# Kernel tuning notes

Measured on AMD Instinct MI355X. Metric: run time of the kernel, lower is better.

The kernel has to match this reference:

```python
import jax, jax.numpy as jnp
import numpy as np
import math

D_MODEL = 1024
N_HEADS = 16
N_QUBITS = 8
HEAD_DIM = D_MODEL // N_HEADS
B, L = 2, 2048


def setup_inputs() -> dict:
    key = jax.random.key(0)
    ks = jax.random.split(key, 16)
    s = 0.02
    return {
        "query": jax.random.normal(ks[0], (B, L, D_MODEL), jnp.float32),
        "key_": jax.random.normal(ks[1], (B, L, D_MODEL), jnp.float32),
        "value": jax.random.normal(ks[2], (B, L, D_MODEL), jnp.float32),
        "Wq": jax.random.normal(ks[3], (D_MODEL, D_MODEL), jnp.float32) * s,
        "bq": jnp.zeros((D_MODEL,), jnp.float32),
        "Wk": jax.random.normal(ks[4], (D_MODEL, D_MODEL), jnp.float32) * s,
        "bk": jnp.zeros((D_MODEL,), jnp.float32),
        "Wv": jax.random.normal(ks[5], (D_MODEL, D_MODEL), jnp.float32) * s,
        "bv": jnp.zeros((D_MODEL,), jnp.float32),
        "Wo": jax.random.normal(ks[6], (D_MODEL, D_MODEL), jnp.float32) * s,
        "bo": jnp.zeros((D_MODEL,), jnp.float32),
        "Wf": jax.random.normal(ks[7], (HEAD_DIM, N_QUBITS), jnp.float32) * s,  # feature map weight (input->qubits)
        "bf": jnp.zeros((N_QUBITS,), jnp.float32),
        "quantum_weights": jax.random.normal(ks[8], (N_HEADS, N_QUBITS), jnp.float32) * 0.1,
        "entanglement_strength": jnp.asarray(0.5, jnp.float32),
    }


def _heads(x):
    # [B, L, D] -> [B, H, L, head_dim]
    b, l, _ = x.shape
    return x.reshape(b, l, N_HEADS, HEAD_DIM).transpose(0, 2, 1, 3)


def reference(query, key_, value, Wq, bq, Wk, bk, Wv, bv, Wo, bo, Wf, bf, quantum_weights, entanglement_strength):
    Qh = _heads(query @ Wq.T + bq)   # [B,H,L,d]
    Kh = _heads(key_ @ Wk.T + bk)
    Vh = _heads(value @ Wv.T + bv)

    classical = jnp.einsum("bhid,bhjd->bhij", Qh, Kh) / math.sqrt(HEAD_DIM)

    # quantum feature map: tanh(linear) -> [B,H,L,Q]
    qq = jnp.tanh(jnp.einsum("bhld,dq->bhlq", Qh, Wf) + bf)
    kq = jnp.tanh(jnp.einsum("bhld,dq->bhlq", Kh, Wf) + bf)

    # mean_q w_q*cos(qq_i - kq_j) == (1/Q)[(w*cos qq)@cos(kq)^T + (w*sin qq)@sin(kq)^T]
    w = jax.nn.sigmoid(quantum_weights)[None, :, None, :]  # [1,H,1,Q]
    quantum = (
        jnp.einsum("bhiq,bhjq->bhij", jnp.cos(qq) * w, jnp.cos(kq))
        + jnp.einsum("bhiq,bhjq->bhij", jnp.sin(qq) * w, jnp.sin(kq))
    ) / N_QUBITS
    ent = jax.nn.sigmoid(entanglement_strength)
    quantum = quantum * ent

    mix = ent  # same sigmoid(entanglement_strength) used as mixing weight
    combined = (1.0 - mix) * classical + mix * quantum

    attn = jax.nn.softmax(combined, axis=-1)  # [B,H,L,L]
    attended = jnp.einsum("bhij,bhjd->bhid", attn, Vh)
    attended = attended.transpose(0, 2, 1, 3).reshape(query.shape[0], query.shape[1], D_MODEL)
    output = attended @ Wo.T + bo
    return output, attn.mean(axis=1)
```

## Files before the change

### kernel.cpp

```cpp
#include <hip/hip_runtime.h>


typedef unsigned short u16;
typedef unsigned int u32;
typedef short v8s __attribute__((ext_vector_type(8)));
typedef float v4f __attribute__((ext_vector_type(4)));

static __device__ __forceinline__ float b2f(u16 h) {
  union { u32 u; float f; } a; a.u = ((u32)h) << 16; return a.f;
}
static __device__ __forceinline__ u16 f2b(float f) {
  union { float f; u32 u; } a; a.f = f;
  u32 u = a.u;
  u32 r = u + 0x7FFFu + ((u >> 16) & 1u);
  return (u16)(r >> 16);
}
static __device__ __forceinline__ u32 fbits(float f) {
  union { float f; u32 u; } a; a.f = f; return a.u;
}
static __device__ __forceinline__ v4f mfma16(v8s a, v8s b, v4f c) {
  return __builtin_amdgcn_mfma_f32_16x16x32_bf16(a, b, c, 0, 0, 0);
}
static __device__ __forceinline__ void gload16(const u16* g, u16* l) {
  __builtin_amdgcn_global_load_lds((const __attribute__((address_space(1))) u32*)g,
                                   (__attribute__((address_space(3))) u32*)l, 16, 0, 0);
}

__global__ __launch_bounds__(256) void k_f2b(const float* __restrict__ x, u16* __restrict__ y, int n4) {
  int i = blockIdx.x * 256 + threadIdx.x;
  if (i >= n4) return;
  float4 v = ((const float4*)x)[i];
  union { u16 s[4]; uint2 u; } o;
  o.s[0] = f2b(v.x); o.s[1] = f2b(v.y); o.s[2] = f2b(v.z); o.s[3] = f2b(v.w);
  ((uint2*)y)[i] = o.u;
}

__global__ __launch_bounds__(256) void k_gemm128(
    const u16* __restrict__ A0, const u16* __restrict__ A1, const u16* __restrict__ A2,
    const u16* __restrict__ B0, const u16* __restrict__ B1, const u16* __restrict__ B2,
    const float* __restrict__ bias0, const float* __restrict__ bias1, const float* __restrict__ bias2,
    u16* __restrict__ O0, u16* __restrict__ O1, u16* __restrict__ O2t,
    float* __restrict__ Cf) {
  __shared__ __align__(16) u16 As[128 * 32];
  __shared__ __align__(16) u16 Bs[128 * 32];
  __shared__ __align__(16) u16 Ts[4][64][68];
  const int K = 1024, N = 1024;
  int t = threadIdx.x, w = t >> 6, lane = t & 63, quad = lane >> 4, l16 = lane & 15;
  int z = blockIdx.z;
  const u16* A = (z == 0) ? A0 : (z == 1) ? A1 : A2;
  const u16* Bm = (z == 0) ? B0 : (z == 1) ? B1 : B2;
  const float* bias = (z == 0) ? bias0 : (z == 1) ? bias1 : bias2;
  int n0 = blockIdx.x * 128, m0 = blockIdx.y * 128;

  int srow = lane >> 2, scol = (lane & 3) * 8;
  const u16 *ga[2], *gb[2];
  u16 *la[2], *lbp[2];
#pragma unroll
  for (int p = 0; p < 2; ++p) {
    int row = p * 64 + w * 16 + srow;
    ga[p] = A + (size_t)(m0 + row) * K + scol;
    gb[p] = Bm + (size_t)(n0 + row) * K + scol;
    la[p] = As + (p * 256 + w * 64) * 8;
    lbp[p] = Bs + (p * 256 + w * 64) * 8;
  }

  int mrow = (w >> 1) * 64, ncol = (w & 1) * 64;
  v4f zf = {0.f, 0.f, 0.f, 0.f};
  v4f acc[4][4];
#pragma unroll
  for (int mi = 0; mi < 4; ++mi)
#pragma unroll
    for (int ni = 0; ni < 4; ++ni) acc[mi][ni] = zf;

  for (int k0 = 0; k0 < K; k0 += 32) {
    __syncthreads();
#pragma unroll
    for (int p = 0; p < 2; ++p) {
      gload16(ga[p] + k0, la[p]);
      gload16(gb[p] + k0, lbp[p]);
    }
    __syncthreads();
    v8s af[4], bfr[4];
#pragma unroll
    for (int x = 0; x < 4; ++x) {
      af[x] = *(const v8s*)&As[(mrow + x * 16 + l16) * 32 + quad * 8];
      bfr[x] = *(const v8s*)&Bs[(ncol + x * 16 + l16) * 32 + quad * 8];
    }
#pragma unroll
    for (int mi = 0; mi < 4; ++mi)
#pragma unroll
      for (int ni = 0; ni < 4; ++ni)
        acc[mi][ni] = mfma16(af[mi], bfr[ni], acc[mi][ni]);
  }

  float bv[4];
#pragma unroll
  for (int ni = 0; ni < 4; ++ni) bv[ni] = bias[n0 + ncol + ni * 16 + l16];

  if (Cf) {
#pragma unroll
    for (int mi = 0; mi < 4; ++mi)
#pragma unroll
      for (int ni = 0; ni < 4; ++ni)
#pragma unroll
        for (int r = 0; r < 4; ++r)
          Cf[(size_t)(m0 + mrow + mi * 16 + quad * 4 + r) * N + n0 + ncol + ni * 16 + l16] =
              acc[mi][ni][r] + bv[ni];
  } else if (z != 2) {
    u16* O = z ? O1 : O0;
#pragma unroll
    for (int mi = 0; mi < 4; ++mi)
#pragma unroll
      for (int ni = 0; ni < 4; ++ni)
#pragma unroll
        for (int r = 0; r < 4; ++r)
          O[(size_t)(m0 + mrow + mi * 16 + quad * 4 + r) * N + n0 + ncol + ni * 16 + l16] =
              f2b(acc[mi][ni][r] + bv[ni]);
  } else {
#pragma unroll
    for (int mi = 0; mi < 4; ++mi)
#pragma unroll
      for (int ni = 0; ni < 4; ++ni)
#pragma unroll
        for (int r = 0; r < 4; ++r)
          Ts[w][mi * 16 + quad * 4 + r][ni * 16 + l16] = f2b(acc[mi][ni][r] + bv[ni]);
    int c = lane;
    union { uint4 u[8]; u16 s[64]; } cb;
#pragma unroll
    for (int e = 0; e < 64; ++e) cb.s[e] = Ts[w][e][c];
    int bb = m0 >> 11, ml = m0 & 2047;
    u16* dst = O2t + ((size_t)(bb * 1024 + n0 + ncol + c)) * 2048 + ml + mrow;
#pragma unroll
    for (int e = 0; e < 8; ++e) *(uint4*)(dst + e * 8) = cb.u[e];
  }
}

__global__ __launch_bounds__(256) void k_features(const u16* __restrict__ P, const float* __restrict__ Wf,
                                                  const float* __restrict__ bff, const float* __restrict__ qw,
                                                  const float* __restrict__ entp, u16* __restrict__ Out, int isK) {
  int idx = blockIdx.x * 256 + threadIdx.x;
  int b = idx >> 15, h = (idx >> 11) & 15, l = idx & 2047;
  const u16* src = P + ((size_t)(b * 2048 + l)) * 1024 + h * 64;
  u16* dst = Out + (size_t)idx * 96;
  float x[64];
#pragma unroll
  for (int g = 0; g < 8; ++g) {
    union { uint4 u; u16 s[8]; } uu;
    uu.u = *(const uint4*)(src + g * 8);
#pragma unroll
    for (int e = 0; e < 8; ++e) x[g * 8 + e] = b2f(uu.s[e]);
  }
  float qv[8];
#pragma unroll
  for (int q = 0; q < 8; ++q) {
    float a = bff[q];
    for (int d = 0; d < 64; ++d) a += x[d] * Wf[d * 8 + q];
    qv[q] = tanhf(a);
  }
  float ent = 1.f / (1.f + __expf(-entp[0]));
  if (!isK) {
#pragma unroll
    for (int g = 0; g < 8; ++g) *(uint4*)(dst + g * 8) = *(const uint4*)(src + g * 8);
#pragma unroll
    for (int q = 0; q < 8; ++q) {
      float sw = 1.f / (1.f + __expf(-qw[h * 8 + q]));
      dst[64 + q] = f2b(cosf(qv[q]) * sw);
      dst[72 + q] = f2b(sinf(qv[q]) * sw);
    }
  } else {
    float c1 = (1.f - ent) * 0.125f, c2 = ent * ent * 0.125f;
#pragma unroll
    for (int d = 0; d < 64; ++d) dst[d] = f2b(x[d] * c1);
#pragma unroll
    for (int q = 0; q < 8; ++q) {
      dst[64 + q] = f2b(cosf(qv[q]) * c2);
      dst[72 + q] = f2b(sinf(qv[q]) * c2);
    }
  }
#pragma unroll
  for (int e = 80; e < 96; ++e) dst[e] = 0;
}

__global__ __launch_bounds__(256) void k_flash(const u16* __restrict__ Qa, const u16* __restrict__ Ka,
                                               const u16* __restrict__ VtG, u16* __restrict__ At,
                                               float* __restrict__ lb) {
  __shared__ __align__(16) u16 Ks[64][104];
  __shared__ __align__(16) u16 Vt[64][72];
  __shared__ __align__(16) u16 Ps[4][2][16][72];

  int t = threadIdx.x, w = t >> 6, lane = t & 63, quad = lane >> 4, l16 = lane & 15;
  int i0 = blockIdx.x * 128, h = blockIdx.y, b = blockIdx.z;
  size_t qbase = ((size_t)(b * 16 + h)) * 2048 * 96;
  v8s aq[2][3];
#pragma unroll
  for (int i16 = 0; i16 < 2; ++i16) {
    const u16* Qrow = Qa + qbase + (size_t)(i0 + w * 32 + i16 * 16 + l16) * 96;
#pragma unroll
    for (int ks = 0; ks < 3; ++ks) aq[i16][ks] = *(const v8s*)(Qrow + ks * 32 + quad * 8);
  }
  const u16* Kbase = Ka + qbase;
  const u16* Vbase = VtG + ((size_t)(b * 1024 + h * 64)) * 2048;

  const u16 *kg[3], *vg[2];
  u16 *kd[3], *vd[2];
#pragma unroll
  for (int p = 0; p < 3; ++p) {
    int idx = t + p * 256, r_ = idx / 12, c_ = idx % 12;
    kg[p] = Kbase + (size_t)r_ * 96 + c_ * 8;
    kd[p] = &Ks[r_][c_ * 8];
  }
#pragma unroll
  for (int p = 0; p < 2; ++p) {
    int idx = t + p * 256, d_ = idx >> 3, c_ = (idx & 7) * 8;
    vg[p] = Vbase + (size_t)d_ * 2048 + c_;
    vd[p] = &Vt[d_][c_];
  }

  v4f zf = {0.f, 0.f, 0.f, 0.f};
  v4f oacc[2][4];
#pragma unroll
  for (int i16 = 0; i16 < 2; ++i16)
#pragma unroll
    for (int d16 = 0; d16 < 4; ++d16) oacc[i16][d16] = zf;
  float l_acc[2] = {0.f, 0.f};

  uint4 fk0 = *(const uint4*)kg[0];
  uint4 fk1 = *(const uint4*)kg[1];
  uint4 fk2 = *(const uint4*)kg[2];
  uint4 fv0 = *(const uint4*)vg[0];
  uint4 fv1 = *(const uint4*)vg[1];

  for (int j0 = 0; j0 < 2048; j0 += 64) {
    *(uint4*)kd[0] = fk0;
    *(uint4*)kd[1] = fk1;
    *(uint4*)kd[2] = fk2;
    *(uint4*)vd[0] = fv0;
    *(uint4*)vd[1] = fv1;
    __syncthreads();
    kg[0] += 6144; kg[1] += 6144; kg[2] += 6144; vg[0] += 64; vg[1] += 64;
    if (j0 + 64 < 2048) {
      fk0 = *(const uint4*)kg[0];
      fk1 = *(const uint4*)kg[1];
      fk2 = *(const uint4*)kg[2];
      fv0 = *(const uint4*)vg[0];
      fv1 = *(const uint4*)vg[1];
    }

    v4f sacc[2][4];
#pragma unroll
    for (int i16 = 0; i16 < 2; ++i16)
#pragma unroll
      for (int j16 = 0; j16 < 4; ++j16) sacc[i16][j16] = zf;
#pragma unroll
    for (int j16 = 0; j16 < 4; ++j16)
#pragma unroll
      for (int ks = 0; ks < 3; ++ks) {
        v8s kf = *(const v8s*)&Ks[j16 * 16 + l16][ks * 32 + quad * 8];
        sacc[0][j16] = mfma16(kf, aq[0][ks], sacc[0][j16]);
        sacc[1][j16] = mfma16(kf, aq[1][ks], sacc[1][j16]);
      }

#pragma unroll
    for (int i16 = 0; i16 < 2; ++i16)
#pragma unroll
      for (int j16 = 0; j16 < 4; ++j16) {
        float e0 = __expf(sacc[i16][j16][0]);
        float e1 = __expf(sacc[i16][j16][1]);
        float e2 = __expf(sacc[i16][j16][2]);
        float e3 = __expf(sacc[i16][j16][3]);
        l_acc[i16] += (e0 + e1) + (e2 + e3);
        uint2 pp;
        pp.x = __builtin_amdgcn_perm(fbits(e1) + 0x8000u, fbits(e0) + 0x8000u, 0x07060302u);
        pp.y = __builtin_amdgcn_perm(fbits(e3) + 0x8000u, fbits(e2) + 0x8000u, 0x07060302u);
        *(uint2*)&Ps[w][i16][l16][j16 * 16 + quad * 4] = pp;
      }
#pragma unroll
    for (int jh = 0; jh < 2; ++jh) {
      v8s pf0 = *(const v8s*)&Ps[w][0][l16][jh * 32 + quad * 8];
      v8s pf1 = *(const v8s*)&Ps[w][1][l16][jh * 32 + quad * 8];
#pragma unroll
      for (int d16 = 0; d16 < 4; ++d16) {
        v8s vf = *(const v8s*)&Vt[d16 * 16 + l16][jh * 32 + quad * 8];
        oacc[0][d16] = mfma16(pf0, vf, oacc[0][d16]);
        oacc[1][d16] = mfma16(pf1, vf, oacc[1][d16]);
      }
    }
    __syncthreads();
  }

#pragma unroll
  for (int i16 = 0; i16 < 2; ++i16) {
    l_acc[i16] += __shfl_xor(l_acc[i16], 16, 64);
    l_acc[i16] += __shfl_xor(l_acc[i16], 32, 64);
    float linv = 1.f / l_acc[i16];
#pragma unroll
    for (int r = 0; r < 4; ++r) {
      float li = __shfl(linv, quad * 4 + r, 64);
      int ri = i0 + w * 32 + i16 * 16 + quad * 4 + r;
#pragma unroll
      for (int d16 = 0; d16 < 4; ++d16)
        At[((size_t)(b * 2048 + ri)) * 1024 + h * 64 + d16 * 16 + l16] = f2b(oacc[i16][d16][r] * li);
    }
    if (lane < 16) {
      size_t mbase = ((size_t)(b * 16 + h)) * 2048;
      lb[mbase + i0 + w * 32 + i16 * 16 + lane] = l_acc[i16];
    }
  }
}

__global__ __launch_bounds__(256) void k_pass2(const u16* __restrict__ Qa, const u16* __restrict__ Ka,
                                               const float* __restrict__ lb,
                                               float* __restrict__ out1) {
  __shared__ __align__(16) u16 Ks[64][104];
  __shared__ float Ls[16][128];
  int t = threadIdx.x, w = t >> 6, lane = t & 63, quad = lane >> 4, l16 = lane & 15;
  int j0 = blockIdx.x * 64, i0 = blockIdx.y * 128, b = blockIdx.z;

#pragma unroll
  for (int rep = 0; rep < 8; ++rep) {
    int idx = t + rep * 256;
    int hh = idx >> 7, il = idx & 127;
    Ls[hh][il] = 0.0625f / lb[((size_t)(b * 16 + hh)) * 2048 + i0 + il];
  }

  size_t base0 = (size_t)b * 16 * 2048 * 96;
  const u16* kg[3]; u16* kd[3];
#pragma unroll
  for (int rep = 0; rep < 3; ++rep) {
    int idx = t + rep * 256;
    int r_ = idx / 12, c_ = idx % 12;
    kg[rep] = Ka + base0 + (size_t)(j0 + r_) * 96 + c_ * 8;
    kd[rep] = &Ks[r_][c_ * 8];
  }
  uint4 f0 = *(const uint4*)kg[0];
  uint4 f1 = *(const uint4*)kg[1];
  uint4 f2 = *(const uint4*)kg[2];

  const u16* q0 = Qa + base0 + (size_t)(i0 + w * 32 + l16) * 96 + quad * 8;
  const u16* q1 = q0 + 16 * 96;

  v4f zf = {0.f, 0.f, 0.f, 0.f};
  v4f macc[2][4];
#pragma unroll
  for (int i16 = 0; i16 < 2; ++i16)
#pragma unroll
    for (int j16 = 0; j16 < 4; ++j16) macc[i16][j16] = zf;

  v8s a[2][3];
#pragma unroll
  for (int ks = 0; ks < 3; ++ks) {
    a[0][ks] = *(const v8s*)(q0 + ks * 32);
    a[1][ks] = *(const v8s*)(q1 + ks * 32);
  }

  for (int h = 0; h < 16; ++h) {
    *(uint4*)kd[0] = f0;
    *(uint4*)kd[1] = f1;
    *(uint4*)kd[2] = f2;
    __syncthreads();
    if (h < 15) {
      kg[0] += 196608; kg[1] += 196608; kg[2] += 196608;
      f0 = *(const uint4*)kg[0];
      f1 = *(const uint4*)kg[1];
      f2 = *(const uint4*)kg[2];
    }

    v4f sacc[2][4];
#pragma unroll
    for (int i16 = 0; i16 < 2; ++i16)
#pragma unroll
      for (int j16 = 0; j16 < 4; ++j16) sacc[i16][j16] = zf;
#pragma unroll
    for (int ks = 0; ks < 3; ++ks)
#pragma unroll
      for (int j16 = 0; j16 < 4; ++j16) {
        v8s kf = *(const v8s*)&Ks[j16 * 16 + l16][ks * 32 + quad * 8];
        sacc[0][j16] = mfma16(a[0][ks], kf, sacc[0][j16]);
        sacc[1][j16] = mfma16(a[1][ks], kf, sacc[1][j16]);
      }

    if (h < 15) {
      q0 += 196608; q1 += 196608;
#pragma unroll
      for (int ks = 0; ks < 3; ++ks) {
        a[0][ks] = *(const v8s*)(q0 + ks * 32);
        a[1][ks] = *(const v8s*)(q1 + ks * 32);
      }
    }

    float li[2][4];
#pragma unroll
    for (int i16 = 0; i16 < 2; ++i16)
#pragma unroll
      for (int r = 0; r < 4; ++r)
        li[i16][r] = Ls[h][w * 32 + i16 * 16 + quad * 4 + r];
#pragma unroll
    for (int i16 = 0; i16 < 2; ++i16)
#pragma unroll
      for (int j16 = 0; j16 < 4; ++j16)
#pragma unroll
        for (int r = 0; r < 4; ++r)
          macc[i16][j16][r] += __expf(sacc[i16][j16][r]) * li[i16][r];
    __syncthreads();
  }

  float* o = out1 + (size_t)b * 2048 * 2048;
#pragma unroll
  for (int i16 = 0; i16 < 2; ++i16)
#pragma unroll
    for (int j16 = 0; j16 < 4; ++j16)
#pragma unroll
      for (int r = 0; r < 4; ++r)
        o[(size_t)(i0 + w * 32 + i16 * 16 + quad * 4 + r) * 2048 + j0 + j16 * 16 + l16] =
            macc[i16][j16][r];
}

extern "C" void kernel_launch(void* const* d_in, const int* in_sizes, int n_in,
                              void* d_out, int out_size, void* d_ws, size_t ws_size,
                              hipStream_t stream) {
  (void)in_sizes; (void)n_in; (void)out_size; (void)ws_size;
  const float* query = (const float*)d_in[0];
  const float* key_  = (const float*)d_in[1];
  const float* value = (const float*)d_in[2];
  const float* Wq = (const float*)d_in[3];
  const float* bq = (const float*)d_in[4];
  const float* Wk = (const float*)d_in[5];
  const float* bk = (const float*)d_in[6];
  const float* Wv = (const float*)d_in[7];
  const float* bv = (const float*)d_in[8];
  const float* Wo = (const float*)d_in[9];
  const float* bo = (const float*)d_in[10];
  const float* Wf = (const float*)d_in[11];
  const float* bff = (const float*)d_in[12];
  const float* qw = (const float*)d_in[13];
  const float* entp = (const float*)d_in[14];

  char* p = (char*)d_ws;
  u16* Xq  = (u16*)(p + 0);
  u16* Xk  = (u16*)(p + 8388608);
  u16* Xv  = (u16*)(p + 16777216);
  u16* Wqb = (u16*)(p + 25165824);
  u16* Wkb = (u16*)(p + 27262976);
  u16* Wvb = (u16*)(p + 29360128);
  u16* Wob = (u16*)(p + 31457280);
  u16* Qp  = (u16*)(p + 33554432);
  u16* Kp  = (u16*)(p + 41943040);
  u16* VtG = (u16*)(p + 50331648);
  u16* Qaa = (u16*)(p + 58720256);
  u16* Kaa = (u16*)(p + 71303168);
  float* lb = (float*)(p + 84148224);
  u16* At  = (u16*)(p + 84410368);

  k_f2b<<<4096, 256, 0, stream>>>(query, Xq, 1048576);
  k_f2b<<<4096, 256, 0, stream>>>(key_,  Xk, 1048576);
  k_f2b<<<4096, 256, 0, stream>>>(value, Xv, 1048576);
  k_f2b<<<1024, 256, 0, stream>>>(Wq, Wqb, 262144);
  k_f2b<<<1024, 256, 0, stream>>>(Wk, Wkb, 262144);
  k_f2b<<<1024, 256, 0, stream>>>(Wv, Wvb, 262144);
  k_f2b<<<1024, 256, 0, stream>>>(Wo, Wob, 262144);

  k_gemm128<<<dim3(8, 32, 3), 256, 0, stream>>>(Xq, Xk, Xv, Wqb, Wkb, Wvb, bq, bk, bv,
                                                Qp, Kp, VtG, nullptr);

  k_features<<<256, 256, 0, stream>>>(Qp, Wf, bff, qw, entp, Qaa, 0);
  k_features<<<256, 256, 0, stream>>>(Kp, Wf, bff, qw, entp, Kaa, 1);

  k_flash<<<dim3(16, 16, 2), 256, 0, stream>>>(Qaa, Kaa, VtG, At, lb);

  k_pass2<<<dim3(32, 16, 2), 256, 0, stream>>>(Qaa, Kaa, lb, (float*)d_out + 4194304);

  k_gemm128<<<dim3(8, 32, 1), 256, 0, stream>>>(At, At, At, Wob, Wob, Wob, bo, bo, bo,
                                                nullptr, nullptr, nullptr, (float*)d_out);
}
```

Measured before the change: 359.9 us.

## Merge conversion launches, deepen GEMM K-step, double-buffer flash K and register V

The seven fp32-to-bf16 conversion launches become one kernel that writes a contiguous workspace, and the Q and K feature launches become one 2D launch. The GEMM now loads a 64-wide K slab per barrier pair and reuses the staging LDS for the transpose epilogue. The feature kernel vectorises the Wf matvec, computes tanh via exp with fast sincos, and writes 16-byte stores. Flash attention double-buffers K in LDS and keeps V fragments in registers loaded straight from global memory, which removes one barrier per tile but raises register pressure.

```diff
diff --git a/kernel.cpp b/kernel.cpp
--- a/kernel.cpp
+++ b/kernel.cpp
@@ -26,12 +26,22 @@
                                    (__attribute__((address_space(3))) u32*)l, 16, 0, 0);
 }
 
-__global__ __launch_bounds__(256) void k_f2b(const float* __restrict__ x, u16* __restrict__ y, int n4) {
+__global__ __launch_bounds__(256) void k_f2b_all(const float* __restrict__ q, const float* __restrict__ k,
+                                                 const float* __restrict__ v, const float* __restrict__ wq,
+                                                 const float* __restrict__ wk, const float* __restrict__ wv,
+                                                 const float* __restrict__ wo, u16* __restrict__ y) {
   int i = blockIdx.x * 256 + threadIdx.x;
-  if (i >= n4) return;
-  float4 v = ((const float4*)x)[i];
+  const float* src; int off;
+  if (i < 1048576)      { src = q;  off = i; }
+  else if (i < 2097152) { src = k;  off = i - 1048576; }
+  else if (i < 3145728) { src = v;  off = i - 2097152; }
+  else if (i < 3407872) { src = wq; off = i - 3145728; }
+  else if (i < 3670016) { src = wk; off = i - 3407872; }
+  else if (i < 3932160) { src = wv; off = i - 3670016; }
+  else                  { src = wo; off = i - 3932160; }
+  float4 val = ((const float4*)src)[off];
   union { u16 s[4]; uint2 u; } o;
-  o.s[0] = f2b(v.x); o.s[1] = f2b(v.y); o.s[2] = f2b(v.z); o.s[3] = f2b(v.w);
+  o.s[0] = f2b(val.x); o.s[1] = f2b(val.y); o.s[2] = f2b(val.z); o.s[3] = f2b(val.w);
   ((uint2*)y)[i] = o.u;
 }
 
@@ -41,9 +51,9 @@
     const float* __restrict__ bias0, const float* __restrict__ bias1, const float* __restrict__ bias2,
     u16* __restrict__ O0, u16* __restrict__ O1, u16* __restrict__ O2t,
     float* __restrict__ Cf) {
-  __shared__ __align__(16) u16 As[128 * 32];
-  __shared__ __align__(16) u16 Bs[128 * 32];
-  __shared__ __align__(16) u16 Ts[4][64][68];
+  __shared__ __align__(16) u16 pool[18432];
+  u16* As = pool;
+  u16* Bs = pool + 8192;
   const int K = 1024, N = 1024;
   int t = threadIdx.x, w = t >> 6, lane = t & 63, quad = lane >> 4, l16 = lane & 15;
   int z = blockIdx.z;
@@ -53,15 +63,13 @@
   int n0 = blockIdx.x * 128, m0 = blockIdx.y * 128;
 
   int srow = lane >> 2, scol = (lane & 3) * 8;
-  const u16 *ga[2], *gb[2];
-  u16 *la[2], *lbp[2];
-#pragma unroll
-  for (int p = 0; p < 2; ++p) {
-    int row = p * 64 + w * 16 + srow;
-    ga[p] = A + (size_t)(m0 + row) * K + scol;
-    gb[p] = Bm + (size_t)(n0 + row) * K + scol;
-    la[p] = As + (p * 256 + w * 64) * 8;
-    lbp[p] = Bs + (p * 256 + w * 64) * 8;
+  const u16* gp[8]; u16* lp[8];
+#pragma unroll
+  for (int qi = 0; qi < 8; ++qi) {
+    int mat = qi >> 2, kk = (qi >> 1) & 1, g = w + (qi & 1) * 4;
+    int row = g * 16 + srow;
+    gp[qi] = (mat ? Bm + (size_t)(n0 + row) * K : A + (size_t)(m0 + row) * K) + kk * 32 + scol;
+    lp[qi] = (mat ? Bs : As) + kk * 4096 + g * 512;
   }
 
   int mrow = (w >> 1) * 64, ncol = (w & 1) * 64;
@@ -72,25 +80,25 @@
 #pragma unroll
     for (int ni = 0; ni < 4; ++ni) acc[mi][ni] = zf;
 
-  for (int k0 = 0; k0 < K; k0 += 32) {
+  for (int k0 = 0; k0 < K; k0 += 64) {
     __syncthreads();
 #pragma unroll
-    for (int p = 0; p < 2; ++p) {
-      gload16(ga[p] + k0, la[p]);
-      gload16(gb[p] + k0, lbp[p]);
-    }
+    for (int qi = 0; qi < 8; ++qi) gload16(gp[qi] + k0, lp[qi]);
     __syncthreads();
-    v8s af[4], bfr[4];
-#pragma unroll
-    for (int x = 0; x < 4; ++x) {
-      af[x] = *(const v8s*)&As[(mrow + x * 16 + l16) * 32 + quad * 8];
-      bfr[x] = *(const v8s*)&Bs[(ncol + x * 16 + l16) * 32 + quad * 8];
-    }
-#pragma unroll
-    for (int mi = 0; mi < 4; ++mi)
-#pragma unroll
-      for (int ni = 0; ni < 4; ++ni)
-        acc[mi][ni] = mfma16(af[mi], bfr[ni], acc[mi][ni]);
+#pragma unroll
+    for (int kk = 0; kk < 2; ++kk) {
+      v8s af[4], bfr[4];
+#pragma unroll
+      for (int x = 0; x < 4; ++x) {
+        af[x] = *(const v8s*)&As[kk * 4096 + (mrow + x * 16 + l16) * 32 + quad * 8];
+        bfr[x] = *(const v8s*)&Bs[kk * 4096 + (ncol + x * 16 + l16) * 32 + quad * 8];
+      }
+#pragma unroll
+      for (int mi = 0; mi < 4; ++mi)
+#pragma unroll
+        for (int ni = 0; ni < 4; ++ni)
+          acc[mi][ni] = mfma16(af[mi], bfr[ni], acc[mi][ni]);
+    }
   }
 
   float bv[4];
@@ -117,17 +125,19 @@
           O[(size_t)(m0 + mrow + mi * 16 + quad * 4 + r) * N + n0 + ncol + ni * 16 + l16] =
               f2b(acc[mi][ni][r] + bv[ni]);
   } else {
+    __syncthreads();
+    u16* Ts = pool + w * 64 * 68;
 #pragma unroll
     for (int mi = 0; mi < 4; ++mi)
 #pragma unroll
       for (int ni = 0; ni < 4; ++ni)
 #pragma unroll
         for (int r = 0; r < 4; ++r)
-          Ts[w][mi * 16 + quad * 4 + r][ni * 16 + l16] = f2b(acc[mi][ni][r] + bv[ni]);
+          Ts[(mi * 16 + quad * 4 + r) * 68 + ni * 16 + l16] = f2b(acc[mi][ni][r] + bv[ni]);
     int c = lane;
     union { uint4 u[8]; u16 s[64]; } cb;
 #pragma unroll
-    for (int e = 0; e < 64; ++e) cb.s[e] = Ts[w][e][c];
+    for (int e = 0; e < 64; ++e) cb.s[e] = Ts[e * 68 + c];
     int bb = m0 >> 11, ml = m0 & 2047;
     u16* dst = O2t + ((size_t)(bb * 1024 + n0 + ncol + c)) * 2048 + ml + mrow;
 #pragma unroll
@@ -135,13 +145,19 @@
   }
 }
 
-__global__ __launch_bounds__(256) void k_features(const u16* __restrict__ P, const float* __restrict__ Wf,
-                                                  const float* __restrict__ bff, const float* __restrict__ qw,
-                                                  const float* __restrict__ entp, u16* __restrict__ Out, int isK) {
+__global__ __launch_bounds__(256) void k_features(const u16* __restrict__ Qp, const u16* __restrict__ Kp,
+                                                  const float* __restrict__ Wf, const float* __restrict__ bff,
+                                                  const float* __restrict__ qw, const float* __restrict__ entp,
+                                                  u16* __restrict__ Qaa, u16* __restrict__ Kaa) {
+  int isK = blockIdx.y;
+  const u16* P = isK ? Kp : Qp;
+  u16* Out = isK ? Kaa : Qaa;
   int idx = blockIdx.x * 256 + threadIdx.x;
   int b = idx >> 15, h = (idx >> 11) & 15, l = idx & 2047;
   const u16* src = P + ((size_t)(b * 2048 + l)) * 1024 + h * 64;
   u16* dst = Out + (size_t)idx * 96;
+  const float4* Wf4 = (const float4*)Wf;
+
   float x[64];
 #pragma unroll
   for (int g = 0; g < 8; ++g) {
@@ -152,40 +168,58 @@
   }
   float qv[8];
 #pragma unroll
-  for (int q = 0; q < 8; ++q) {
-    float a = bff[q];
-    for (int d = 0; d < 64; ++d) a += x[d] * Wf[d * 8 + q];
-    qv[q] = tanhf(a);
+  for (int qq = 0; qq < 8; ++qq) qv[qq] = bff[qq];
+#pragma unroll
+  for (int d = 0; d < 64; ++d) {
+    float4 wa = Wf4[d * 2], wb = Wf4[d * 2 + 1];
+    float xd = x[d];
+    qv[0] += xd * wa.x; qv[1] += xd * wa.y; qv[2] += xd * wa.z; qv[3] += xd * wa.w;
+    qv[4] += xd * wb.x; qv[5] += xd * wb.y; qv[6] += xd * wb.z; qv[7] += xd * wb.w;
+  }
+  float cs[8], sn[8];
+#pragma unroll
+  for (int qq = 0; qq < 8; ++qq) {
+    float e2 = __expf(2.f * qv[qq]);
+    float th = 1.f - 2.f / (e2 + 1.f);
+    __sincosf(th, &sn[qq], &cs[qq]);
   }
   float ent = 1.f / (1.f + __expf(-entp[0]));
+  union { uint4 u; u16 s[8]; } pc, ps;
   if (!isK) {
 #pragma unroll
     for (int g = 0; g < 8; ++g) *(uint4*)(dst + g * 8) = *(const uint4*)(src + g * 8);
 #pragma unroll
-    for (int q = 0; q < 8; ++q) {
-      float sw = 1.f / (1.f + __expf(-qw[h * 8 + q]));
-      dst[64 + q] = f2b(cosf(qv[q]) * sw);
-      dst[72 + q] = f2b(sinf(qv[q]) * sw);
+    for (int qq = 0; qq < 8; ++qq) {
+      float sw = 1.f / (1.f + __expf(-qw[h * 8 + qq]));
+      pc.s[qq] = f2b(cs[qq] * sw);
+      ps.s[qq] = f2b(sn[qq] * sw);
     }
   } else {
     float c1 = (1.f - ent) * 0.125f, c2 = ent * ent * 0.125f;
 #pragma unroll
-    for (int d = 0; d < 64; ++d) dst[d] = f2b(x[d] * c1);
-#pragma unroll
-    for (int q = 0; q < 8; ++q) {
-      dst[64 + q] = f2b(cosf(qv[q]) * c2);
-      dst[72 + q] = f2b(sinf(qv[q]) * c2);
-    }
-  }
-#pragma unroll
-  for (int e = 80; e < 96; ++e) dst[e] = 0;
+    for (int g = 0; g < 8; ++g) {
+      union { uint4 u; u16 s[8]; } ob;
+#pragma unroll
+      for (int e = 0; e < 8; ++e) ob.s[e] = f2b(x[g * 8 + e] * c1);
+      *(uint4*)(dst + g * 8) = ob.u;
+    }
+#pragma unroll
+    for (int qq = 0; qq < 8; ++qq) {
+      pc.s[qq] = f2b(cs[qq] * c2);
+      ps.s[qq] = f2b(sn[qq] * c2);
+    }
+  }
+  *(uint4*)(dst + 64) = pc.u;
+  *(uint4*)(dst + 72) = ps.u;
+  uint4 z4 = {0, 0, 0, 0};
+  *(uint4*)(dst + 80) = z4;
+  *(uint4*)(dst + 88) = z4;
 }
 
 __global__ __launch_bounds__(256) void k_flash(const u16* __restrict__ Qa, const u16* __restrict__ Ka,
                                                const u16* __restrict__ VtG, u16* __restrict__ At,
                                                float* __restrict__ lb) {
-  __shared__ __align__(16) u16 Ks[64][104];
-  __shared__ __align__(16) u16 Vt[64][72];
+  __shared__ __align__(16) u16 Ks[2][64][104];
   __shared__ __align__(16) u16 Ps[4][2][16][72];
 
   int t = threadIdx.x, w = t >> 6, lane = t & 63, quad = lane >> 4, l16 = lane & 15;
@@ -201,20 +235,15 @@
   const u16* Kbase = Ka + qbase;
   const u16* Vbase = VtG + ((size_t)(b * 1024 + h * 64)) * 2048;
 
-  const u16 *kg[3], *vg[2];
-  u16 *kd[3], *vd[2];
+  const u16* kg[3]; int kdo[3];
 #pragma unroll
   for (int p = 0; p < 3; ++p) {
     int idx = t + p * 256, r_ = idx / 12, c_ = idx % 12;
     kg[p] = Kbase + (size_t)r_ * 96 + c_ * 8;
-    kd[p] = &Ks[r_][c_ * 8];
-  }
-#pragma unroll
-  for (int p = 0; p < 2; ++p) {
-    int idx = t + p * 256, d_ = idx >> 3, c_ = (idx & 7) * 8;
-    vg[p] = Vbase + (size_t)d_ * 2048 + c_;
-    vd[p] = &Vt[d_][c_];
-  }
+    kdo[p] = r_ * 104 + c_ * 8;
+  }
+  u16* ks0 = &Ks[0][0][0];
+  u16* ks1 = &Ks[1][0][0];
 
   v4f zf = {0.f, 0.f, 0.f, 0.f};
   v4f oacc[2][4];
@@ -227,23 +256,42 @@
   uint4 fk0 = *(const uint4*)kg[0];
   uint4 fk1 = *(const uint4*)kg[1];
   uint4 fk2 = *(const uint4*)kg[2];
-  uint4 fv0 = *(const uint4*)vg[0];
-  uint4 fv1 = *(const uint4*)vg[1];
+  kg[0] += 6144; kg[1] += 6144; kg[2] += 6144;
+  *(uint4*)(ks0 + kdo[0]) = fk0;
+  *(uint4*)(ks0 + kdo[1]) = fk1;
+  *(uint4*)(ks0 + kdo[2]) = fk2;
+  fk0 = *(const uint4*)kg[0];
+  fk1 = *(const uint4*)kg[1];
+  fk2 = *(const uint4*)kg[2];
+  kg[0] += 6144; kg[1] += 6144; kg[2] += 6144;
+  v8s vf[8];
+#pragma unroll
+  for (int idx = 0; idx < 8; ++idx)
+    vf[idx] = *(const v8s*)(Vbase + (size_t)((idx >> 1) * 16 + l16) * 2048 + (idx & 1) * 32 + quad * 8);
+  __syncthreads();
 
   for (int j0 = 0; j0 < 2048; j0 += 64) {
-    *(uint4*)kd[0] = fk0;
-    *(uint4*)kd[1] = fk1;
-    *(uint4*)kd[2] = fk2;
-    *(uint4*)vd[0] = fv0;
-    *(uint4*)vd[1] = fv1;
-    __syncthreads();
-    kg[0] += 6144; kg[1] += 6144; kg[2] += 6144; vg[0] += 64; vg[1] += 64;
-    if (j0 + 64 < 2048) {
+    int cur = (j0 >> 6) & 1;
+    const u16* kb = cur ? ks1 : ks0;
+    u16* kw = cur ? ks0 : ks1;
+    bool more = (j0 + 64) < 2048;
+    if (more) {
+      *(uint4*)(kw + kdo[0]) = fk0;
+      *(uint4*)(kw + kdo[1]) = fk1;
+      *(uint4*)(kw + kdo[2]) = fk2;
+    }
+    if (j0 + 128 < 2048) {
       fk0 = *(const uint4*)kg[0];
       fk1 = *(const uint4*)kg[1];
       fk2 = *(const uint4*)kg[2];
-      fv0 = *(const uint4*)vg[0];
-      fv1 = *(const uint4*)vg[1];
+      kg[0] += 6144; kg[1] += 6144; kg[2] += 6144;
+    }
+    v8s vn[8];
+    if (more) {
+#pragma unroll
+      for (int idx = 0; idx < 8; ++idx)
+        vn[idx] = *(const v8s*)(Vbase + (size_t)((idx >> 1) * 16 + l16) * 2048 + j0 + 64 +
+                                (idx & 1) * 32 + quad * 8);
     }
 
     v4f sacc[2][4];
@@ -255,7 +303,7 @@
     for (int j16 = 0; j16 < 4; ++j16)
 #pragma unroll
       for (int ks = 0; ks < 3; ++ks) {
-        v8s kf = *(const v8s*)&Ks[j16 * 16 + l16][ks * 32 + quad * 8];
+        v8s kf = *(const v8s*)(kb + (j16 * 16 + l16) * 104 + ks * 32 + quad * 8);
         sacc[0][j16] = mfma16(kf, aq[0][ks], sacc[0][j16]);
         sacc[1][j16] = mfma16(kf, aq[1][ks], sacc[1][j16]);
       }
@@ -280,12 +328,16 @@
       v8s pf1 = *(const v8s*)&Ps[w][1][l16][jh * 32 + quad * 8];
 #pragma unroll
       for (int d16 = 0; d16 < 4; ++d16) {
-        v8s vf = *(const v8s*)&Vt[d16 * 16 + l16][jh * 32 + quad * 8];
-        oacc[0][d16] = mfma16(pf0, vf, oacc[0][d16]);
-        oacc[1][d16] = mfma16(pf1, vf, oacc[1][d16]);
+        v8s vv = vf[d16 * 2 + jh];
+        oacc[0][d16] = mfma16(pf0, vv, oacc[0][d16]);
+        oacc[1][d16] = mfma16(pf1, vv, oacc[1][d16]);
       }
     }
-    __syncthreads();
+    if (more) {
+#pragma unroll
+      for (int idx = 0; idx < 8; ++idx) vf[idx] = vn[idx];
+      __syncthreads();
+    }
   }
 
 #pragma unroll
@@ -442,7 +494,6 @@
   u16* Wqb = (u16*)(p + 25165824);
   u16* Wkb = (u16*)(p + 27262976);
   u16* Wvb = (u16*)(p + 29360128);
-  u16* Wob = (u16*)(p + 31457280);
   u16* Qp  = (u16*)(p + 33554432);
   u16* Kp  = (u16*)(p + 41943040);
   u16* VtG = (u16*)(p + 50331648);
@@ -450,20 +501,14 @@
   u16* Kaa = (u16*)(p + 71303168);
   float* lb = (float*)(p + 84148224);
   u16* At  = (u16*)(p + 84410368);
-
-  k_f2b<<<4096, 256, 0, stream>>>(query, Xq, 1048576);
-  k_f2b<<<4096, 256, 0, stream>>>(key_,  Xk, 1048576);
-  k_f2b<<<4096, 256, 0, stream>>>(value, Xv, 1048576);
-  k_f2b<<<1024, 256, 0, stream>>>(Wq, Wqb, 262144);
-  k_f2b<<<1024, 256, 0, stream>>>(Wk, Wkb, 262144);
-  k_f2b<<<1024, 256, 0, stream>>>(Wv, Wvb, 262144);
-  k_f2b<<<1024, 256, 0, stream>>>(Wo, Wob, 262144);
+  u16* Wob = (u16*)(p + 31457280);
+
+  k_f2b_all<<<16384, 256, 0, stream>>>(query, key_, value, Wq, Wk, Wv, Wo, Xq);
 
   k_gemm128<<<dim3(8, 32, 3), 256, 0, stream>>>(Xq, Xk, Xv, Wqb, Wkb, Wvb, bq, bk, bv,
                                                 Qp, Kp, VtG, nullptr);
 
-  k_features<<<256, 256, 0, stream>>>(Qp, Wf, bff, qw, entp, Qaa, 0);
-  k_features<<<256, 256, 0, stream>>>(Kp, Wf, bff, qw, entp, Kaa, 1);
+  k_features<<<dim3(256, 2), 256, 0, stream>>>(Qp, Kp, Wf, bff, qw, entp, Qaa, Kaa);
 
   k_flash<<<dim3(16, 16, 2), 256, 0, stream>>>(Qaa, Kaa, VtG, At, lb);
 
```

After: 352.3 us. -2.1%, faster.
